# Optimization experiments

Hardware: AMD Instinct MI355X
Metric: run time of the kernel (lower is better)

The kernel has to match this reference:

```python
import jax, jax.numpy as jnp
import numpy as np

B, S, D = 2, 2048, 7168
R, H, VD = 1024, 16, 128
QK_HD = R // H            # 64, per-head latent q/k dim
SCALE = float(np.sqrt(D // H))  # self.scale = d_heads ** 0.5 = sqrt(448)


def setup_inputs() -> dict:
    key = jax.random.key(0)
    ks = jax.random.split(key, 6)
    return {
        "x":   jax.random.normal(ks[0], (B, S, D), dtype=jnp.float32),
        "Wq":  jax.random.normal(ks[1], (R, D), dtype=jnp.float32) * 0.02,
        "Wkv": jax.random.normal(ks[2], (R, D), dtype=jnp.float32) * 0.02,
        "Wvb": jax.random.normal(ks[3], (H * VD, R), dtype=jnp.float32) * 0.02,
        "Wo":  jax.random.normal(ks[4], (D, H * VD), dtype=jnp.float32) * 0.02,
        "bo":  jnp.zeros((D,), dtype=jnp.float32),
    }


def reference(x, Wq, Wkv, Wvb, Wo, bo):
    b, s, d = x.shape
    # low-rank compressed projections (torch Linear: y = x @ W.T)
    q_lat  = x @ Wq.T            # [B,S,R] compressed query
    kv_lat = x @ Wkv.T           # [B,S,R] compressed KV latent (shared K)
    q = q_lat.reshape(b, s, H, QK_HD)    # [B,S,H,64]
    k = kv_lat.reshape(b, s, H, QK_HD)   # [B,S,H,64]
    # up-project values from latent
    v = (kv_lat @ Wvb.T).reshape(b, s, H, VD)  # [B,S,H,128]
    # scaled causal attention in latent head space
    scores = jnp.einsum("bqhd,bkhd->bhqk", q, k) / SCALE  # [B,H,S,S]
    causal = jnp.tril(jnp.ones((s, s), dtype=bool))
    scores = jnp.where(causal, scores, jnp.finfo(scores.dtype).min)
    attn = jax.nn.softmax(scores, axis=-1)
    out = jnp.einsum("bhqk,bkhd->bqhd", attn, v).reshape(b, s, H * VD)
    return out @ Wo.T + bo       # [B,S,D]
```

## Files before the change

kernel.cpp:

```cpp
#include <hip/hip_runtime.h>
#include <hip/hip_bf16.h>

typedef __bf16 bf16_t;
typedef __attribute__((ext_vector_type(8))) __bf16 bf16x8;
typedef __attribute__((ext_vector_type(4))) __bf16 bf16x4;
typedef __attribute__((ext_vector_type(4))) float f32x4;

#define B_ 2
#define S_ 2048
#define D_ 7168
#define R_ 1024
#define H_ 16
#define VD_ 128
#define MROWS 4096
#define NQKV 2048
#define HVD 2048

__device__ __forceinline__ void gload_lds16(const bf16_t* g, bf16_t* l) {
    __builtin_amdgcn_global_load_lds(
        (const __attribute__((address_space(1))) unsigned int*)(g),
        (__attribute__((address_space(3))) unsigned int*)(l),
        16, 0, 0);
}

__global__ __launch_bounds__(256)
void cvt_f32_bf16(const float* __restrict__ src, bf16_t* __restrict__ dst, float scale) {
    size_t i = ((size_t)blockIdx.x * 256 + threadIdx.x) * 4;
    f32x4 v = *(const f32x4*)(src + i);
    bf16x4 o;
    o[0] = (bf16_t)(v[0] * scale);
    o[1] = (bf16_t)(v[1] * scale);
    o[2] = (bf16_t)(v[2] * scale);
    o[3] = (bf16_t)(v[3] * scale);
    *(bf16x4*)(dst + i) = o;
}

template<int OUTF32>
__global__ __launch_bounds__(256)
void gemm_bt(const bf16_t* __restrict__ A, int lda,
             const bf16_t* __restrict__ Bt, int ldb,
             void* __restrict__ Cv, int ldc,
             const float* __restrict__ bias, int K)
{
    __shared__ __align__(16) bf16_t As[2][128 * 64];
    __shared__ __align__(16) bf16_t Bs[2][128 * 64];
    const int tid  = threadIdx.x;
    const int lane = tid & 63;
    const int wave = tid >> 6;
    const int tileM = blockIdx.y * 128;
    const int tileN = blockIdx.x * 128;
    const int wr = (wave >> 1) * 64;
    const int wc = (wave & 1) * 64;
    const int r  = lane & 15;
    const int kq = lane >> 4;

    const bf16_t* Ag = A  + (size_t)tileM * lda;
    const bf16_t* Bg = Bt + (size_t)tileN * ldb;

    int srow[4], scol[4], slin[4];
    #pragma unroll
    for (int i = 0; i < 4; ++i) {
        slin[i] = (i * 256 + tid) * 8;
        srow[i] = slin[i] >> 6;
        scol[i] = (slin[i] & 63) ^ ((srow[i] & 7) << 3);
    }

    #define ISSUE_TILE(buf, k0)                                                  \
        {                                                                        \
            _Pragma("unroll")                                                    \
            for (int i = 0; i < 4; ++i) {                                        \
                gload_lds16(Ag + (size_t)srow[i] * lda + (k0) + scol[i], As[buf] + slin[i]); \
                gload_lds16(Bg + (size_t)srow[i] * ldb + (k0) + scol[i], Bs[buf] + slin[i]); \
            }                                                                    \
        }

    f32x4 acc[4][4] = {};
    const int nt = K >> 6;

    ISSUE_TILE(0, 0)
    ISSUE_TILE(1, 64)
    asm volatile("s_waitcnt vmcnt(8)" ::: "memory");
    __builtin_amdgcn_s_barrier();
    __builtin_amdgcn_sched_barrier(0);

    for (int t = 0; t < nt; ++t) {
        const int cur = t & 1;
        const bf16_t* Ab = As[cur];
        const bf16_t* Bb = Bs[cur];

        bf16x8 af[4][2], bfr[4][2];
        #pragma unroll
        for (int m = 0; m < 4; ++m)
            #pragma unroll
            for (int kk = 0; kk < 2; ++kk) {
                const int e = (wr + m * 16 + r) * 64 + kk * 32 + kq * 8;
                af[m][kk] = *(const bf16x8*)(Ab + (e ^ ((r & 7) << 3)));
            }
        #pragma unroll
        for (int n = 0; n < 4; ++n)
            #pragma unroll
            for (int kk = 0; kk < 2; ++kk) {
                const int e = (wc + n * 16 + r) * 64 + kk * 32 + kq * 8;
                bfr[n][kk] = *(const bf16x8*)(Bb + (e ^ ((r & 7) << 3)));
            }
        #pragma unroll
        for (int kk = 0; kk < 2; ++kk)
            #pragma unroll
            for (int m = 0; m < 4; ++m)
                #pragma unroll
                for (int n = 0; n < 4; ++n)
                    acc[m][n] = __builtin_amdgcn_mfma_f32_16x16x32_bf16(af[m][kk], bfr[n][kk], acc[m][n], 0, 0, 0);

        __builtin_amdgcn_s_barrier();
        __builtin_amdgcn_sched_barrier(0);
        if (t + 2 < nt) {
            ISSUE_TILE(cur, (t + 2) << 6)
            asm volatile("s_waitcnt vmcnt(8)" ::: "memory");
        } else {
            asm volatile("s_waitcnt vmcnt(0)" ::: "memory");
        }
        __builtin_amdgcn_s_barrier();
        __builtin_amdgcn_sched_barrier(0);
    }
    #undef ISSUE_TILE

    const int orow = tileM + wr + kq * 4;
    const int ocol = tileN + wc + r;
    if (OUTF32) {
        float* C = (float*)Cv;
        #pragma unroll
        for (int n = 0; n < 4; ++n) {
            float bv = bias[ocol + n * 16];
            #pragma unroll
            for (int m = 0; m < 4; ++m)
                #pragma unroll
                for (int j = 0; j < 4; ++j)
                    C[(size_t)(orow + m * 16 + j) * ldc + ocol + n * 16] = acc[m][n][j] + bv;
        }
    } else {
        bf16_t* C = (bf16_t*)Cv;
        #pragma unroll
        for (int m = 0; m < 4; ++m)
            #pragma unroll
            for (int n = 0; n < 4; ++n)
                #pragma unroll
                for (int j = 0; j < 4; ++j)
                    C[(size_t)(orow + m * 16 + j) * ldc + ocol + n * 16] = (bf16_t)acc[m][n][j];
    }
}

#define LOADK(KF, kvb_)                                                          \
    {                                                                            \
        _Pragma("unroll")                                                        \
        for (int n = 0; n < 4; ++n) {                                            \
            const bf16_t* kp_ = Kp + (size_t)((kvb_) + n * 16 + r) * NQKV + kq * 8; \
            KF[n][0] = *(const bf16x8*)kp_;                                      \
            KF[n][1] = *(const bf16x8*)(kp_ + 32);                               \
        }                                                                        \
    }

#define QKMM(KF)                                                                 \
    {                                                                            \
        _Pragma("unroll")                                                        \
        for (int n = 0; n < 4; ++n)                                              \
            _Pragma("unroll")                                                    \
            for (int m = 0; m < 2; ++m) {                                        \
                s[m][n] = __builtin_amdgcn_mfma_f32_16x16x32_bf16(qf[m][0], KF[n][0], s[m][n], 0, 0, 0); \
                s[m][n] = __builtin_amdgcn_mfma_f32_16x16x32_bf16(qf[m][1], KF[n][1], s[m][n], 0, 0, 0); \
            }                                                                    \
    }

__device__ __forceinline__ void attn_qtile32(
    const bf16_t* __restrict__ Q, const bf16_t* __restrict__ Kp,
    const bf16_t* __restrict__ Vp, bf16_t* __restrict__ Op,
    bf16_t* __restrict__ P_lds, int qbase, int lane)
{
    const int r  = lane & 15;
    const int kq = lane >> 4;

    bf16x8 qf[2][2];
    #pragma unroll
    for (int m = 0; m < 2; ++m)
        #pragma unroll
        for (int kk = 0; kk < 2; ++kk)
            qf[m][kk] = *(const bf16x8*)(Q + (size_t)(qbase + m * 16 + r) * NQKV + kk * 32 + kq * 8);

    f32x4 o[2][8] = {};
    float mst[2][4], lst[2][4];
    #pragma unroll
    for (int m = 0; m < 2; ++m)
        #pragma unroll
        for (int j = 0; j < 4; ++j) { mst[m][j] = -INFINITY; lst[m][j] = 0.0f; }

    const int nfull  = qbase >> 6;
    const int ntiles = (qbase + 95) >> 6;

    bf16x8 kfA[4][2], kfB[4][2];
    LOADK(kfA, 0)

    for (int t = 0; t < ntiles; ++t) {
        const int kvb = t * 64;
        const bool useA = ((t & 1) == 0);
        f32x4 s[2][4] = {};
        if (useA) { QKMM(kfA) } else { QKMM(kfB) }
        if (t + 1 < ntiles) {
            const int nk = (t + 1) * 64;
            if (useA) { LOADK(kfB, nk) } else { LOADK(kfA, nk) }
        }
        if (t >= nfull) {
            #pragma unroll
            for (int m = 0; m < 2; ++m)
                #pragma unroll
                for (int n = 0; n < 4; ++n)
                    #pragma unroll
                    for (int j = 0; j < 4; ++j) {
                        int kc = kvb + n * 16 + r;
                        int qr = qbase + m * 16 + kq * 4 + j;
                        if (kc > qr) s[m][n][j] = -1e30f;
                    }
        }
        float mx[2][4];
        #pragma unroll
        for (int m = 0; m < 2; ++m)
            #pragma unroll
            for (int j = 0; j < 4; ++j) {
                float v = fmaxf(fmaxf(s[m][0][j], s[m][1][j]), fmaxf(s[m][2][j], s[m][3][j]));
                #pragma unroll
                for (int d = 1; d < 16; d <<= 1) v = fmaxf(v, __shfl_xor(v, d, 64));
                mx[m][j] = v;
            }
        bool need = false;
        #pragma unroll
        for (int m = 0; m < 2; ++m)
            #pragma unroll
            for (int j = 0; j < 4; ++j) need |= (mx[m][j] > mst[m][j] + 8.0f);
        if (__ballot(need)) {
            #pragma unroll
            for (int m = 0; m < 2; ++m)
                #pragma unroll
                for (int j = 0; j < 4; ++j) {
                    float mnew  = fmaxf(mst[m][j], mx[m][j]);
                    float alpha = __expf(mst[m][j] - mnew);
                    lst[m][j] *= alpha;
                    mst[m][j]  = mnew;
                    #pragma unroll
                    for (int n = 0; n < 8; ++n) o[m][n][j] *= alpha;
                }
        }
        #pragma unroll
        for (int m = 0; m < 2; ++m)
            #pragma unroll
            for (int j = 0; j < 4; ++j) {
                float rs = 0.0f;
                const int row = m * 16 + kq * 4 + j;
                #pragma unroll
                for (int n = 0; n < 4; ++n) {
                    float pv = __expf(s[m][n][j] - mst[m][j]);
                    rs += pv;
                    const int c = (n * 16 + r) ^ ((row & 7) << 3);
                    P_lds[row * 64 + c] = (bf16_t)pv;
                }
                #pragma unroll
                for (int d = 1; d < 16; d <<= 1) rs += __shfl_xor(rs, d, 64);
                lst[m][j] += rs;
            }
        bf16x8 pf[2][2];
        #pragma unroll
        for (int m = 0; m < 2; ++m)
            #pragma unroll
            for (int kk = 0; kk < 2; ++kk) {
                const int e = (m * 16 + r) * 64 + kk * 32 + kq * 8;
                pf[m][kk] = *(const bf16x8*)(P_lds + (e ^ ((r & 7) << 3)));
            }
        #pragma unroll
        for (int n = 0; n < 8; ++n) {
            #pragma unroll
            for (int kk = 0; kk < 2; ++kk) {
                bf16x8 vf = *(const bf16x8*)(Vp + (size_t)(n * 16 + r) * MROWS + kvb + kk * 32 + kq * 8);
                #pragma unroll
                for (int m = 0; m < 2; ++m)
                    o[m][n] = __builtin_amdgcn_mfma_f32_16x16x32_bf16(pf[m][kk], vf, o[m][n], 0, 0, 0);
            }
        }
    }

    #pragma unroll
    for (int m = 0; m < 2; ++m)
        #pragma unroll
        for (int j = 0; j < 4; ++j) {
            float inv = 1.0f / lst[m][j];
            int row = m * 16 + kq * 4 + j;
            #pragma unroll
            for (int n = 0; n < 8; ++n)
                Op[(size_t)(qbase + row) * HVD + n * 16 + r] = (bf16_t)(o[m][n][j] * inv);
        }
}

__global__ __launch_bounds__(64, 1)
void attn_kernel(const bf16_t* __restrict__ qkv, const bf16_t* __restrict__ Vt,
                 bf16_t* __restrict__ O)
{
    __shared__ __align__(16) bf16_t P_lds[32 * 64];
    const int lane = threadIdx.x;
    const int p = blockIdx.x;
    const int h = blockIdx.y;
    const int b = blockIdx.z;

    const bf16_t* Q  = qkv + (size_t)(b * S_) * NQKV + h * 64;
    const bf16_t* Kp = qkv + (size_t)(b * S_) * NQKV + R_ + h * 64;
    const bf16_t* Vp = Vt + (size_t)(h * VD_) * MROWS + b * S_;
    bf16_t* Op = O + (size_t)(b * S_) * HVD + h * VD_;

    attn_qtile32(Q, Kp, Vp, Op, P_lds, (63 - p) * 32, lane);
    attn_qtile32(Q, Kp, Vp, Op, P_lds, p * 32, lane);
}

extern "C" void kernel_launch(void* const* d_in, const int* in_sizes, int n_in,
                              void* d_out, int out_size, void* d_ws, size_t ws_size,
                              hipStream_t stream) {
    const float* x   = (const float*)d_in[0];
    const float* Wq  = (const float*)d_in[1];
    const float* Wkv = (const float*)d_in[2];
    const float* Wvb = (const float*)d_in[3];
    const float* Wo  = (const float*)d_in[4];
    const float* bo  = (const float*)d_in[5];

    char* oc = (char*)d_out;
    bf16_t* xb     = (bf16_t*)oc;
    bf16_t* Wqkv_b = (bf16_t*)(oc + 58720256);
    char* ws = (char*)d_ws;
    bf16_t* qkv_b  = (bf16_t*)ws;
    bf16_t* Wvb_b  = (bf16_t*)(ws + 16777216);
    bf16_t* Vt_b   = (bf16_t*)(ws + 20971520);
    bf16_t* attn_b = (bf16_t*)(ws + 37748736);
    bf16_t* Wo_b   = (bf16_t*)(ws + 54525952);

    const float inv_scale = 0.047245559f;

    cvt_f32_bf16<<<29360128 / 1024, 256, 0, stream>>>(x,   xb, 1.0f);
    cvt_f32_bf16<<< 7340032 / 1024, 256, 0, stream>>>(Wq,  Wqkv_b, inv_scale);
    cvt_f32_bf16<<< 7340032 / 1024, 256, 0, stream>>>(Wkv, Wqkv_b + 7340032, 1.0f);
    cvt_f32_bf16<<< 2097152 / 1024, 256, 0, stream>>>(Wvb, Wvb_b, 1.0f);
    cvt_f32_bf16<<<14680064 / 1024, 256, 0, stream>>>(Wo,  Wo_b, 1.0f);

    gemm_bt<0><<<dim3(16, 32), 256, 0, stream>>>(xb, D_, Wqkv_b, D_, qkv_b, NQKV, nullptr, D_);
    gemm_bt<0><<<dim3(32, 16), 256, 0, stream>>>(Wvb_b, R_, qkv_b + R_, NQKV, Vt_b, MROWS, nullptr, R_);
    attn_kernel<<<dim3(32, H_, B_), 64, 0, stream>>>(qkv_b, Vt_b, attn_b);
    gemm_bt<1><<<dim3(56, 32), 256, 0, stream>>>(attn_b, HVD, Wo_b, HVD, d_out, D_, bo, HVD);
}
```

Baseline: 602.1 us.

## Drop K double-buffering in attention, add GEMM MFMA priority and LDS barriers

```diff
diff --git a/kernel.cpp b/kernel.cpp
--- a/kernel.cpp
+++ b/kernel.cpp
@@ -103,6 +103,7 @@
                 const int e = (wc + n * 16 + r) * 64 + kk * 32 + kq * 8;
                 bfr[n][kk] = *(const bf16x8*)(Bb + (e ^ ((r & 7) << 3)));
             }
+        __builtin_amdgcn_s_setprio(1);
         #pragma unroll
         for (int kk = 0; kk < 2; ++kk)
             #pragma unroll
@@ -110,6 +111,7 @@
                 #pragma unroll
                 for (int n = 0; n < 4; ++n)
                     acc[m][n] = __builtin_amdgcn_mfma_f32_16x16x32_bf16(af[m][kk], bfr[n][kk], acc[m][n], 0, 0, 0);
+        __builtin_amdgcn_s_setprio(0);
 
         __builtin_amdgcn_s_barrier();
         __builtin_amdgcn_sched_barrier(0);
@@ -149,28 +151,7 @@
     }
 }
 
-#define LOADK(KF, kvb_)                                                          \
-    {                                                                            \
-        _Pragma("unroll")                                                        \
-        for (int n = 0; n < 4; ++n) {                                            \
-            const bf16_t* kp_ = Kp + (size_t)((kvb_) + n * 16 + r) * NQKV + kq * 8; \
-            KF[n][0] = *(const bf16x8*)kp_;                                      \
-            KF[n][1] = *(const bf16x8*)(kp_ + 32);                               \
-        }                                                                        \
-    }
-
-#define QKMM(KF)                                                                 \
-    {                                                                            \
-        _Pragma("unroll")                                                        \
-        for (int n = 0; n < 4; ++n)                                              \
-            _Pragma("unroll")                                                    \
-            for (int m = 0; m < 2; ++m) {                                        \
-                s[m][n] = __builtin_amdgcn_mfma_f32_16x16x32_bf16(qf[m][0], KF[n][0], s[m][n], 0, 0, 0); \
-                s[m][n] = __builtin_amdgcn_mfma_f32_16x16x32_bf16(qf[m][1], KF[n][1], s[m][n], 0, 0, 0); \
-            }                                                                    \
-    }
-
-__device__ __forceinline__ void attn_qtile32(
+__device__ __forceinline__ void attn_qtile(
     const bf16_t* __restrict__ Q, const bf16_t* __restrict__ Kp,
     const bf16_t* __restrict__ Vp, bf16_t* __restrict__ Op,
     bf16_t* __restrict__ P_lds, int qbase, int lane)
@@ -195,17 +176,18 @@
     const int nfull  = qbase >> 6;
     const int ntiles = (qbase + 95) >> 6;
 
-    bf16x8 kfA[4][2], kfB[4][2];
-    LOADK(kfA, 0)
-
     for (int t = 0; t < ntiles; ++t) {
         const int kvb = t * 64;
-        const bool useA = ((t & 1) == 0);
         f32x4 s[2][4] = {};
-        if (useA) { QKMM(kfA) } else { QKMM(kfB) }
-        if (t + 1 < ntiles) {
-            const int nk = (t + 1) * 64;
-            if (useA) { LOADK(kfB, nk) } else { LOADK(kfA, nk) }
+        #pragma unroll
+        for (int n = 0; n < 4; ++n) {
+            bf16x8 kf0 = *(const bf16x8*)(Kp + (size_t)(kvb + n * 16 + r) * NQKV + kq * 8);
+            bf16x8 kf1 = *(const bf16x8*)(Kp + (size_t)(kvb + n * 16 + r) * NQKV + 32 + kq * 8);
+            #pragma unroll
+            for (int m = 0; m < 2; ++m) {
+                s[m][n] = __builtin_amdgcn_mfma_f32_16x16x32_bf16(qf[m][0], kf0, s[m][n], 0, 0, 0);
+                s[m][n] = __builtin_amdgcn_mfma_f32_16x16x32_bf16(qf[m][1], kf1, s[m][n], 0, 0, 0);
+            }
         }
         if (t >= nfull) {
             #pragma unroll
@@ -264,6 +246,7 @@
                 for (int d = 1; d < 16; d <<= 1) rs += __shfl_xor(rs, d, 64);
                 lst[m][j] += rs;
             }
+        __syncthreads();
         bf16x8 pf[2][2];
         #pragma unroll
         for (int m = 0; m < 2; ++m)
@@ -282,6 +265,7 @@
                     o[m][n] = __builtin_amdgcn_mfma_f32_16x16x32_bf16(pf[m][kk], vf, o[m][n], 0, 0, 0);
             }
         }
+        __syncthreads();
     }
 
     #pragma unroll
@@ -296,7 +280,7 @@
         }
 }
 
-__global__ __launch_bounds__(64, 1)
+__global__ __launch_bounds__(64)
 void attn_kernel(const bf16_t* __restrict__ qkv, const bf16_t* __restrict__ Vt,
                  bf16_t* __restrict__ O)
 {
@@ -311,8 +295,8 @@
     const bf16_t* Vp = Vt + (size_t)(h * VD_) * MROWS + b * S_;
     bf16_t* Op = O + (size_t)(b * S_) * HVD + h * VD_;
 
-    attn_qtile32(Q, Kp, Vp, Op, P_lds, (63 - p) * 32, lane);
-    attn_qtile32(Q, Kp, Vp, Op, P_lds, p * 32, lane);
+    attn_qtile(Q, Kp, Vp, Op, P_lds, (63 - p) * 32, lane);
+    attn_qtile(Q, Kp, Vp, Op, P_lds, p * 32, lane);
 }
 
 extern "C" void kernel_launch(void* const* d_in, const int* in_sizes, int n_in,
```

Result: faster. 522.8 us (-13.2%).
